# Kernel optimization log

Measured on AMD Instinct MI355X. Metric: run time of the kernel, lower is better.

Reference implementation:

```python
import jax, jax.numpy as jnp
import numpy as np

B, N, D = 8, 8192, 512
WS = 128          # ATTENTION_WINDOW_SIZE
LB = 1            # ATTENTION_WINDOW_LOOKBACK (look_backward)
NW = N // WS      # number of windows (N divisible by WS -> autopad no-op)


def setup_inputs() -> dict:
    key = jax.random.key(0)
    ks = jax.random.split(key, 4)
    s = 0.02
    return {
        "x": jax.random.normal(ks[0], (B, N, D), dtype=jnp.float32),
        "w_q": jax.random.normal(ks[1], (D, D), dtype=jnp.float32) * s,
        "b_q": jnp.zeros((D,), dtype=jnp.float32),
        "w_k": jax.random.normal(ks[2], (D, D), dtype=jnp.float32) * s,
        "b_k": jnp.zeros((D,), dtype=jnp.float32),
        "w_v": jax.random.normal(ks[3], (D, D), dtype=jnp.float32) * s,
        "b_v": jnp.zeros((D,), dtype=jnp.float32),
    }


def _look_around(t, pad_value):
    # t: (B, NW, WS, ...) -> concat of [backward..current] windows along window-length axis
    pad_width = [(0, 0), (LB, 0)] + [(0, 0)] * (t.ndim - 2)
    padded = jnp.pad(t, pad_width, constant_values=pad_value)
    return jnp.concatenate([padded[:, i:i + NW] for i in range(LB + 1)], axis=2)


def _local_attention(q, k, v):
    scale = D ** -0.5
    bq = q.reshape(B, NW, WS, D)
    bk = _look_around(k.reshape(B, NW, WS, D), 0.0)   # (B, NW, (LB+1)*WS, D)
    bv = _look_around(v.reshape(B, NW, WS, D), 0.0)

    # absolute position ticks for causal + padding masks
    tq = jnp.arange(N).reshape(1, NW, WS)                               # query positions
    tk = _look_around(jnp.arange(N).reshape(1, NW, WS), -1)             # key positions, -1 = pad

    sim = jnp.einsum('bwie,bwje->bwij', bq, bk) * scale                 # (B, NW, WS, (LB+1)*WS)
    mask = (tq[..., :, None] < tk[..., None, :]) | (tk[..., None, :] < 0)
    sim = jnp.where(mask, -jnp.finfo(sim.dtype).max, sim)
    attn = jax.nn.softmax(sim, axis=-1)                                  # dropout = 0 -> no-op
    out = jnp.einsum('bwij,bwje->bwie', attn, bv)
    return out.reshape(B, N, D)


def reference(x, w_q, b_q, w_k, b_k, w_v, b_v):
    q = x @ w_q.T + b_q
    k = x @ w_k.T + b_k
    v = x @ w_v.T + b_v
    return _local_attention(q, k, v)
```

## Files before the change

### kernel.cpp

```cpp
#include <hip/hip_runtime.h>


typedef __bf16 bf16x8 __attribute__((ext_vector_type(8)));
typedef float f32x4 __attribute__((ext_vector_type(4)));
typedef unsigned short u16x8 __attribute__((ext_vector_type(8)));

#define BATCH 8
#define SEQ   8192
#define DIM   512
#define NWIN  64
#define TOKS  (BATCH * SEQ)
#define WSELEM ((size_t)TOKS * DIM)

__device__ __forceinline__ unsigned short f2b(float f) {
    union { float f; unsigned int u; } c; c.f = f;
    unsigned int u = c.u;
    return (unsigned short)((u + 0x7FFFu + ((u >> 16) & 1u)) >> 16);
}

__device__ __forceinline__ int swz64(int row, int col) {
    return (row * 64 + col) ^ ((row & 7) << 3);
}
__device__ __forceinline__ int swz128(int row, int col) {
    return (row * 128 + col) ^ ((row & 15) << 3);
}

__device__ __forceinline__ void gload_lds16(const unsigned short* g,
                                            unsigned short* l) {
    __builtin_amdgcn_global_load_lds(
        (const __attribute__((address_space(1))) void*)g,
        (__attribute__((address_space(3))) void*)l, 16, 0, 0);
}

__global__ __launch_bounds__(256) void k_cvt(const float* __restrict__ s,
                                             unsigned short* __restrict__ d,
                                             int n8) {
    const int stride = gridDim.x * blockDim.x;
    for (int i = blockIdx.x * blockDim.x + threadIdx.x; i < n8; i += stride) {
        const float4 a = ((const float4*)s)[2 * i];
        const float4 b = ((const float4*)s)[2 * i + 1];
        u16x8 v;
        v[0] = f2b(a.x); v[1] = f2b(a.y); v[2] = f2b(a.z); v[3] = f2b(a.w);
        v[4] = f2b(b.x); v[5] = f2b(b.y); v[6] = f2b(b.z); v[7] = f2b(b.w);
        ((u16x8*)d)[i] = v;
    }
}

__global__ __launch_bounds__(256, 2) void k_qkv(
    const unsigned short* __restrict__ xb, const unsigned short* __restrict__ wb,
    const float* __restrict__ bq, const float* __restrict__ bk,
    const float* __restrict__ bv,
    unsigned short* __restrict__ qo, unsigned short* __restrict__ ko,
    unsigned short* __restrict__ vto)
{
    __shared__ __align__(16) unsigned short sm[32768];
    unsigned short* Xs = sm;

    int bid = (int)blockIdx.x;
    bid = (bid & 7) * 256 + (bid >> 3);
    const int mt = bid >> 2, nt = bid & 3;
    const int rbase = mt << 7;
    const int cbase = nt << 7;

    const unsigned short* __restrict__ xsrc0 = xb + ((size_t)rbase << 9);
    const unsigned short* __restrict__ wsrc0 = wb + ((size_t)cbase << 9);

    const int tid  = threadIdx.x;
    const int lane = tid & 63;
    const int wid  = tid >> 6;
    const int wm = wid >> 1, wn = wid & 1;
    const int l15 = lane & 15, lg = lane >> 4;

    f32x4 acc[3][4][4];
#pragma unroll
    for (int s = 0; s < 3; ++s)
#pragma unroll
        for (int m = 0; m < 4; ++m)
#pragma unroll
            for (int n = 0; n < 4; ++n) acc[s][m][n] = (f32x4){0.f, 0.f, 0.f, 0.f};

    const int srow = tid >> 3;
    const int gs   = ((tid & 7) ^ (srow & 7)) << 3;
    const int ldso = tid << 3;

    for (int ks = 0; ks < 8; ++ks) {
        const int kc = ks << 6;
#pragma unroll
        for (int i = 0; i < 4; ++i) {
            const int row = (i << 5) + srow;
            gload_lds16(xsrc0 + ((size_t)row << 9) + kc + gs, Xs + (i << 11) + ldso);
        }
#pragma unroll
        for (int ws = 0; ws < 3; ++ws) {
#pragma unroll
            for (int i = 0; i < 4; ++i) {
                const int row = (i << 5) + srow;
                gload_lds16(wsrc0 + ((size_t)ws << 18) + ((size_t)row << 9) + kc + gs,
                            sm + 8192 + (ws << 13) + (i << 11) + ldso);
            }
        }
        __syncthreads();
#pragma unroll
        for (int kk = 0; kk < 64; kk += 32) {
            const int cu = kk + (lg << 3);
            bf16x8 af[4];
#pragma unroll
            for (int m = 0; m < 4; ++m)
                af[m] = *(const bf16x8*)&Xs[swz64((wm << 6) + (m << 4) + l15, cu)];
#pragma unroll
            for (int ws = 0; ws < 3; ++ws) {
                const unsigned short* Wsb = sm + 8192 + (ws << 13);
                bf16x8 bfr[4];
#pragma unroll
                for (int n = 0; n < 4; ++n)
                    bfr[n] = *(const bf16x8*)&Wsb[swz64((wn << 6) + (n << 4) + l15, cu)];
#pragma unroll
                for (int m = 0; m < 4; ++m)
#pragma unroll
                    for (int n = 0; n < 4; ++n)
                        acc[ws][m][n] = __builtin_amdgcn_mfma_f32_16x16x32_bf16(
                            af[m], bfr[n], acc[ws][m][n], 0, 0, 0);
            }
        }
        __syncthreads();
    }

#pragma unroll
    for (int ws = 0; ws < 2; ++ws) {
        unsigned short* __restrict__ out = ws ? ko : qo;
        const float* __restrict__ bias = ws ? bk : bq;
#pragma unroll
        for (int n = 0; n < 4; ++n) {
            const int col = cbase + (wn << 6) + (n << 4) + l15;
            const float bv_ = bias[col];
#pragma unroll
            for (int m = 0; m < 4; ++m)
#pragma unroll
                for (int j = 0; j < 4; ++j) {
                    const int row = rbase + (wm << 6) + (m << 4) + (lg << 2) + j;
                    out[(size_t)row * DIM + col] = f2b(acc[ws][m][n][j] + bv_);
                }
        }
    }
#pragma unroll
    for (int n = 0; n < 4; ++n) {
        const int dv = (wn << 6) + (n << 4) + l15;
        const float bv_ = bv[cbase + dv];
#pragma unroll
        for (int m = 0; m < 4; ++m)
#pragma unroll
            for (int j = 0; j < 4; ++j) {
                const int tok = (wm << 6) + (m << 4) + (lg << 2) + j;
                sm[tok * 129 + dv] = f2b(acc[2][m][n][j] + bv_);
            }
    }
    __syncthreads();
    {
        const int batch = rbase >> 13;
        const int ntok  = rbase & 8191;
        const int dvl0  = tid >> 4;
        const int t16   = (tid & 15) << 3;
#pragma unroll
        for (int p = 0; p < 8; ++p) {
            const int dvl = (p << 4) + dvl0;
            u16x8 v;
#pragma unroll
            for (int j = 0; j < 8; ++j) v[j] = sm[(t16 + j) * 129 + dvl];
            *(u16x8*)&vto[(size_t)batch * (DIM * SEQ)
                          + (size_t)(cbase + dvl) * SEQ + ntok + t16] = v;
        }
    }
}

__global__ __launch_bounds__(512) void k_attn(
    const unsigned short* __restrict__ q,
    const unsigned short* __restrict__ k,
    const unsigned short* __restrict__ vt,
    float* __restrict__ out)
{
    __shared__ __align__(16) unsigned short sm[32768];
    __shared__ float redm[128][4];
    __shared__ float reds[128][4];

    int bid = (int)blockIdx.x;
    bid = (bid & 7) * 64 + (bid >> 3);
    const int b = bid >> 6, w = bid & 63;
    const int tid  = threadIdx.x;
    const int lane = tid & 63, wid = tid >> 6;
    const int l15 = lane & 15, lg = lane >> 4;
    const int wqa = wid >> 2, wka = wid & 3;
    const int kstart = (w - 1) << 7;
    const size_t qrow0 = ((size_t)b << 13) + ((size_t)w << 7);

    f32x4 acc[4][4];
#pragma unroll
    for (int m = 0; m < 4; ++m)
#pragma unroll
        for (int n = 0; n < 4; ++n) acc[m][n] = (f32x4){0.f, 0.f, 0.f, 0.f};

    const int srA = tid >> 4;
    const int gsA = (((tid & 15) ^ (srA & 15)) << 3);

    for (int dstep = 0; dstep < 4; ++dstep) {
        const int dc = dstep << 7;
#pragma unroll
        for (int i = 0; i < 8; ++i) {
            const int r = (i << 5) + srA;
            int krow = kstart + r; krow = krow < 0 ? 0 : krow;
            gload_lds16(k + (((size_t)b << 13) + krow) * DIM + dc + gsA,
                        sm + (i << 12) + (tid << 3));
        }
        __syncthreads();
#pragma unroll
        for (int kk = 0; kk < 128; kk += 32) {
            const int cu = kk + (lg << 3);
            bf16x8 af[4], bf[4];
#pragma unroll
            for (int m = 0; m < 4; ++m) {
                const int rq = (wqa << 6) + (m << 4) + l15;
                af[m] = *(const bf16x8*)&q[(qrow0 + rq) * DIM + dc + cu];
            }
#pragma unroll
            for (int n = 0; n < 4; ++n) {
                const int rk = (wka << 6) + (n << 4) + l15;
                bf[n] = *(const bf16x8*)&sm[swz128(rk, cu)];
            }
#pragma unroll
            for (int m = 0; m < 4; ++m)
#pragma unroll
                for (int n = 0; n < 4; ++n)
                    acc[m][n] = __builtin_amdgcn_mfma_f32_16x16x32_bf16(
                        af[m], bf[n], acc[m][n], 0, 0, 0);
        }
        __syncthreads();
    }

    const float scale = 0.04419417382415922f;
    float pm[4][4];
#pragma unroll
    for (int m = 0; m < 4; ++m)
#pragma unroll
        for (int j = 0; j < 4; ++j) {
            const int qr = (wqa << 6) + (m << 4) + (lg << 2) + j;
            float mx = -3.0e38f;
#pragma unroll
            for (int n = 0; n < 4; ++n) {
                const int c = (wka << 6) + (n << 4) + l15;
                const bool keep = (c <= qr + 128) && (w > 0 || c >= 128);
                const float s = keep ? acc[m][n][j] * scale : -INFINITY;
                acc[m][n][j] = s;
                mx = fmaxf(mx, s);
            }
#pragma unroll
            for (int o = 1; o < 16; o <<= 1) mx = fmaxf(mx, __shfl_xor(mx, o));
            pm[m][j] = mx;
        }
    if (l15 == 0) {
#pragma unroll
        for (int m = 0; m < 4; ++m)
#pragma unroll
            for (int j = 0; j < 4; ++j)
                redm[(wqa << 6) + (m << 4) + (lg << 2) + j][wka] = pm[m][j];
    }
    __syncthreads();

    float ls[4][4];
#pragma unroll
    for (int m = 0; m < 4; ++m)
#pragma unroll
        for (int j = 0; j < 4; ++j) {
            const int qr = (wqa << 6) + (m << 4) + (lg << 2) + j;
            const float g = fmaxf(fmaxf(redm[qr][0], redm[qr][1]),
                                  fmaxf(redm[qr][2], redm[qr][3]));
            float s = 0.f;
#pragma unroll
            for (int n = 0; n < 4; ++n) {
                const float p = __expf(acc[m][n][j] - g);
                acc[m][n][j] = p;
                s += p;
            }
#pragma unroll
            for (int o = 1; o < 16; o <<= 1) s += __shfl_xor(s, o);
            ls[m][j] = s;
        }
    if (l15 == 0) {
#pragma unroll
        for (int m = 0; m < 4; ++m)
#pragma unroll
            for (int j = 0; j < 4; ++j)
                reds[(wqa << 6) + (m << 4) + (lg << 2) + j][wka] = ls[m][j];
    }
    __syncthreads();

#pragma unroll
    for (int m = 0; m < 4; ++m)
#pragma unroll
        for (int j = 0; j < 4; ++j) {
            const int qr = (wqa << 6) + (m << 4) + (lg << 2) + j;
            const float tot = reds[qr][0] + reds[qr][1] + reds[qr][2] + reds[qr][3];
            const float inv = 1.0f / tot;
#pragma unroll
            for (int n = 0; n < 4; ++n) {
                const int c = (wka << 6) + (n << 4) + l15;
                sm[((qr << 8) + c) ^ ((qr & 7) << 3)] = f2b(acc[m][n][j] * inv);
            }
        }
    __syncthreads();

    const int wqb = wid >> 2, wvb = wid & 3;
#pragma unroll
    for (int half = 0; half < 2; ++half) {
        f32x4 oacc[4][4];
#pragma unroll
        for (int m = 0; m < 4; ++m)
#pragma unroll
            for (int n = 0; n < 4; ++n) oacc[m][n] = (f32x4){0.f, 0.f, 0.f, 0.f};
#pragma unroll
        for (int kk = 0; kk < 256; kk += 32) {
            const int klo = kk + (lg << 3);
            bf16x8 af[4], bf[4];
#pragma unroll
            for (int m = 0; m < 4; ++m) {
                const int rq = (wqb << 6) + (m << 4) + l15;
                af[m] = *(const bf16x8*)&sm[((rq << 8) + klo) ^ ((rq & 7) << 3)];
            }
            int key = kstart + klo; key = key < 0 ? 0 : key;
#pragma unroll
            for (int n = 0; n < 4; ++n) {
                const int dv = (half << 8) + (wvb << 6) + (n << 4) + l15;
                bf[n] = *(const bf16x8*)&vt[(((size_t)b * DIM + dv) << 13) + key];
            }
#pragma unroll
            for (int m = 0; m < 4; ++m)
#pragma unroll
                for (int n = 0; n < 4; ++n)
                    oacc[m][n] = __builtin_amdgcn_mfma_f32_16x16x32_bf16(
                        af[m], bf[n], oacc[m][n], 0, 0, 0);
        }
#pragma unroll
        for (int n = 0; n < 4; ++n) {
            const int dv = (half << 8) + (wvb << 6) + (n << 4) + l15;
#pragma unroll
            for (int m = 0; m < 4; ++m)
#pragma unroll
                for (int j = 0; j < 4; ++j) {
                    const int qr = (wqb << 6) + (m << 4) + (lg << 2) + j;
                    out[(qrow0 + qr) * DIM + dv] = oacc[m][n][j];
                }
        }
    }
}

extern "C" void kernel_launch(void* const* d_in, const int* in_sizes, int n_in,
                              void* d_out, int out_size, void* d_ws, size_t ws_size,
                              hipStream_t stream) {
    (void)in_sizes; (void)n_in; (void)out_size; (void)ws_size;
    const float* x  = (const float*)d_in[0];
    const float* wq = (const float*)d_in[1];
    const float* bq = (const float*)d_in[2];
    const float* wk = (const float*)d_in[3];
    const float* bk = (const float*)d_in[4];
    const float* wv = (const float*)d_in[5];
    const float* bv = (const float*)d_in[6];
    float* out = (float*)d_out;

    unsigned short* qws  = (unsigned short*)d_ws;
    unsigned short* kws  = qws + WSELEM;
    unsigned short* vtws = kws + WSELEM;

    unsigned short* xbuf = (unsigned short*)d_out;
    unsigned short* wbuf = xbuf + WSELEM;

    k_cvt<<<2048, 256, 0, stream>>>(x, xbuf, (int)(WSELEM / 8));
    k_cvt<<<128, 256, 0, stream>>>(wq, wbuf, DIM * DIM / 8);
    k_cvt<<<128, 256, 0, stream>>>(wk, wbuf + DIM * DIM, DIM * DIM / 8);
    k_cvt<<<128, 256, 0, stream>>>(wv, wbuf + 2 * DIM * DIM, DIM * DIM / 8);
    k_qkv<<<2048, 256, 0, stream>>>(xbuf, wbuf, bq, bk, bv, qws, kws, vtws);
    k_attn<<<512, 512, 0, stream>>>(qws, kws, vtws, out);
}
```

Measured before the change: 283.3 us.

## Restructure window attention so each wave owns whole query rows, with double-buffered K/V staging

Each wave now computes all 256 key columns for its own 16 query rows. This removes the cross-wave max/sum reductions through shared memory and the barriers that went with them. K tiles are staged into LDS in 64-wide chunks with double buffering. V is written by the projection kernel in a new key-blocked transposed layout, so P·V reads V tiles from double-buffered LDS instead of scattered global loads. Softmax normalization moves to the output store. The risks are heavy register pressure from 128 accumulator floats per lane under launch_bounds(512,2) and a 128 KB LDS footprint.

```diff
diff --git a/kernel.cpp b/kernel.cpp
--- a/kernel.cpp
+++ b/kernel.cpp
@@ -20,9 +20,6 @@
 
 __device__ __forceinline__ int swz64(int row, int col) {
     return (row * 64 + col) ^ ((row & 7) << 3);
-}
-__device__ __forceinline__ int swz128(int row, int col) {
-    return (row * 128 + col) ^ ((row & 15) << 3);
 }
 
 __device__ __forceinline__ void gload_lds16(const unsigned short* g,
@@ -166,21 +163,21 @@
             u16x8 v;
 #pragma unroll
             for (int j = 0; j < 8; ++j) v[j] = sm[(t16 + j) * 129 + dvl];
-            *(u16x8*)&vto[(size_t)batch * (DIM * SEQ)
-                          + (size_t)(cbase + dvl) * SEQ + ntok + t16] = v;
-        }
-    }
-}
-
-__global__ __launch_bounds__(512) void k_attn(
+            const int key0 = ntok + t16;
+            *(u16x8*)&vto[(((size_t)(batch * 256 + (key0 >> 5)) << 9)
+                           + (size_t)(cbase + dvl)) * 32 + (key0 & 31)] = v;
+        }
+    }
+}
+
+__global__ __launch_bounds__(512, 2) void k_attn(
     const unsigned short* __restrict__ q,
     const unsigned short* __restrict__ k,
-    const unsigned short* __restrict__ vt,
+    const unsigned short* __restrict__ vt3,
     float* __restrict__ out)
 {
-    __shared__ __align__(16) unsigned short sm[32768];
-    __shared__ float redm[128][4];
-    __shared__ float reds[128][4];
+    __shared__ __align__(16) unsigned short Kb[32768];
+    __shared__ __align__(16) unsigned short Pl[32768];
 
     int bid = (int)blockIdx.x;
     bid = (bid & 7) * 64 + (bid >> 3);
@@ -188,166 +185,121 @@
     const int tid  = threadIdx.x;
     const int lane = tid & 63, wid = tid >> 6;
     const int l15 = lane & 15, lg = lane >> 4;
-    const int wqa = wid >> 2, wka = wid & 3;
     const int kstart = (w - 1) << 7;
     const size_t qrow0 = ((size_t)b << 13) + ((size_t)w << 7);
-
-    f32x4 acc[4][4];
-#pragma unroll
-    for (int m = 0; m < 4; ++m)
-#pragma unroll
-        for (int n = 0; n < 4; ++n) acc[m][n] = (f32x4){0.f, 0.f, 0.f, 0.f};
-
-    const int srA = tid >> 4;
-    const int gsA = (((tid & 15) ^ (srA & 15)) << 3);
-
-    for (int dstep = 0; dstep < 4; ++dstep) {
-        const int dc = dstep << 7;
-#pragma unroll
-        for (int i = 0; i < 8; ++i) {
-            const int r = (i << 5) + srA;
+    const size_t kbase = (size_t)b << 13;
+
+    const int srow = tid >> 3;
+    const int s0   = tid & 7;
+
+    f32x4 acc[16];
+#pragma unroll
+    for (int n = 0; n < 16; ++n) acc[n] = (f32x4){0.f, 0.f, 0.f, 0.f};
+
+    auto stageK = [&](int buf, int ds) {
+#pragma unroll
+        for (int i = 0; i < 4; ++i) {
+            const int r = (i << 6) + srow;
             int krow = kstart + r; krow = krow < 0 ? 0 : krow;
-            gload_lds16(k + (((size_t)b << 13) + krow) * DIM + dc + gsA,
-                        sm + (i << 12) + (tid << 3));
+            gload_lds16(k + (kbase + krow) * DIM + (ds << 6) + ((s0 ^ (r & 7)) << 3),
+                        Kb + (buf << 14) + (i << 12) + (tid << 3));
+        }
+    };
+
+    stageK(0, 0);
+    stageK(1, 1);
+    __syncthreads();
+    for (int ds = 0; ds < 8; ++ds) {
+        const unsigned short* Kc = Kb + ((ds & 1) << 14);
+#pragma unroll
+        for (int kk2 = 0; kk2 < 2; ++kk2) {
+            const int cu = (kk2 << 5) + (lg << 3);
+            const bf16x8 af = *(const bf16x8*)
+                &q[(qrow0 + (wid << 4) + l15) * DIM + (ds << 6) + cu];
+#pragma unroll
+            for (int n = 0; n < 16; ++n) {
+                const bf16x8 bf = *(const bf16x8*)&Kc[swz64((n << 4) + l15, cu)];
+                acc[n] = __builtin_amdgcn_mfma_f32_16x16x32_bf16(af, bf, acc[n], 0, 0, 0);
+            }
         }
         __syncthreads();
-#pragma unroll
-        for (int kk = 0; kk < 128; kk += 32) {
-            const int cu = kk + (lg << 3);
-            bf16x8 af[4], bf[4];
-#pragma unroll
-            for (int m = 0; m < 4; ++m) {
-                const int rq = (wqa << 6) + (m << 4) + l15;
-                af[m] = *(const bf16x8*)&q[(qrow0 + rq) * DIM + dc + cu];
-            }
-#pragma unroll
-            for (int n = 0; n < 4; ++n) {
-                const int rk = (wka << 6) + (n << 4) + l15;
-                bf[n] = *(const bf16x8*)&sm[swz128(rk, cu)];
-            }
-#pragma unroll
-            for (int m = 0; m < 4; ++m)
-#pragma unroll
-                for (int n = 0; n < 4; ++n)
-                    acc[m][n] = __builtin_amdgcn_mfma_f32_16x16x32_bf16(
-                        af[m], bf[n], acc[m][n], 0, 0, 0);
-        }
-        __syncthreads();
-    }
+        if (ds + 2 < 8) stageK(ds & 1, ds + 2);
+    }
+
+    const int c5base = kstart >> 5;
+    auto stageV = [&](int buf, int kk) {
+        int c5 = c5base + kk; c5 = c5 < 0 ? 0 : c5;
+        const unsigned short* src = vt3 + ((size_t)(b * 256 + c5) << 14);
+#pragma unroll
+        for (int i = 0; i < 4; ++i)
+            gload_lds16(src + (i << 12) + (tid << 3),
+                        Kb + (buf << 14) + (i << 12) + (tid << 3));
+    };
+    stageV(0, 0);
+    stageV(1, 1);
 
     const float scale = 0.04419417382415922f;
-    float pm[4][4];
-#pragma unroll
-    for (int m = 0; m < 4; ++m)
-#pragma unroll
-        for (int j = 0; j < 4; ++j) {
-            const int qr = (wqa << 6) + (m << 4) + (lg << 2) + j;
-            float mx = -3.0e38f;
-#pragma unroll
-            for (int n = 0; n < 4; ++n) {
-                const int c = (wka << 6) + (n << 4) + l15;
-                const bool keep = (c <= qr + 128) && (w > 0 || c >= 128);
-                const float s = keep ? acc[m][n][j] * scale : -INFINITY;
-                acc[m][n][j] = s;
-                mx = fmaxf(mx, s);
-            }
-#pragma unroll
-            for (int o = 1; o < 16; o <<= 1) mx = fmaxf(mx, __shfl_xor(mx, o));
-            pm[m][j] = mx;
-        }
-    if (l15 == 0) {
-#pragma unroll
-        for (int m = 0; m < 4; ++m)
-#pragma unroll
-            for (int j = 0; j < 4; ++j)
-                redm[(wqa << 6) + (m << 4) + (lg << 2) + j][wka] = pm[m][j];
+    float inv[4];
+    unsigned short* Pw = Pl + (wid << 12);
+#pragma unroll
+    for (int jj = 0; jj < 4; ++jj) {
+        const int r  = (lg << 2) + jj;
+        const int qr = (wid << 4) + r;
+        float mx = -3.0e38f;
+#pragma unroll
+        for (int n = 0; n < 16; ++n) {
+            const int c = (n << 4) + l15;
+            const bool keep = (c <= qr + 128) && (w > 0 || c >= 128);
+            const float s = keep ? acc[n][jj] * scale : -INFINITY;
+            acc[n][jj] = s;
+            mx = fmaxf(mx, s);
+        }
+#pragma unroll
+        for (int o = 1; o < 16; o <<= 1) mx = fmaxf(mx, __shfl_xor(mx, o));
+        float sum = 0.f;
+#pragma unroll
+        for (int n = 0; n < 16; ++n) {
+            const float p = __expf(acc[n][jj] - mx);
+            acc[n][jj] = p;
+            sum += p;
+        }
+#pragma unroll
+        for (int o = 1; o < 16; o <<= 1) sum += __shfl_xor(sum, o);
+        inv[jj] = 1.0f / sum;
+#pragma unroll
+        for (int n = 0; n < 16; ++n) {
+            const int c = (n << 4) + l15;
+            Pw[(r << 8) + ((((c >> 3) ^ r) << 3) | (c & 7))] = f2b(acc[n][jj]);
+        }
     }
     __syncthreads();
 
-    float ls[4][4];
-#pragma unroll
-    for (int m = 0; m < 4; ++m)
-#pragma unroll
-        for (int j = 0; j < 4; ++j) {
-            const int qr = (wqa << 6) + (m << 4) + (lg << 2) + j;
-            const float g = fmaxf(fmaxf(redm[qr][0], redm[qr][1]),
-                                  fmaxf(redm[qr][2], redm[qr][3]));
-            float s = 0.f;
-#pragma unroll
-            for (int n = 0; n < 4; ++n) {
-                const float p = __expf(acc[m][n][j] - g);
-                acc[m][n][j] = p;
-                s += p;
-            }
-#pragma unroll
-            for (int o = 1; o < 16; o <<= 1) s += __shfl_xor(s, o);
-            ls[m][j] = s;
-        }
-    if (l15 == 0) {
-#pragma unroll
-        for (int m = 0; m < 4; ++m)
-#pragma unroll
-            for (int j = 0; j < 4; ++j)
-                reds[(wqa << 6) + (m << 4) + (lg << 2) + j][wka] = ls[m][j];
-    }
-    __syncthreads();
-
-#pragma unroll
-    for (int m = 0; m < 4; ++m)
-#pragma unroll
-        for (int j = 0; j < 4; ++j) {
-            const int qr = (wqa << 6) + (m << 4) + (lg << 2) + j;
-            const float tot = reds[qr][0] + reds[qr][1] + reds[qr][2] + reds[qr][3];
-            const float inv = 1.0f / tot;
-#pragma unroll
-            for (int n = 0; n < 4; ++n) {
-                const int c = (wka << 6) + (n << 4) + l15;
-                sm[((qr << 8) + c) ^ ((qr & 7) << 3)] = f2b(acc[m][n][j] * inv);
-            }
-        }
-    __syncthreads();
-
-    const int wqb = wid >> 2, wvb = wid & 3;
-#pragma unroll
-    for (int half = 0; half < 2; ++half) {
-        f32x4 oacc[4][4];
-#pragma unroll
-        for (int m = 0; m < 4; ++m)
-#pragma unroll
-            for (int n = 0; n < 4; ++n) oacc[m][n] = (f32x4){0.f, 0.f, 0.f, 0.f};
-#pragma unroll
-        for (int kk = 0; kk < 256; kk += 32) {
-            const int klo = kk + (lg << 3);
-            bf16x8 af[4], bf[4];
-#pragma unroll
-            for (int m = 0; m < 4; ++m) {
-                const int rq = (wqb << 6) + (m << 4) + l15;
-                af[m] = *(const bf16x8*)&sm[((rq << 8) + klo) ^ ((rq & 7) << 3)];
-            }
-            int key = kstart + klo; key = key < 0 ? 0 : key;
-#pragma unroll
-            for (int n = 0; n < 4; ++n) {
-                const int dv = (half << 8) + (wvb << 6) + (n << 4) + l15;
-                bf[n] = *(const bf16x8*)&vt[(((size_t)b * DIM + dv) << 13) + key];
-            }
-#pragma unroll
-            for (int m = 0; m < 4; ++m)
-#pragma unroll
-                for (int n = 0; n < 4; ++n)
-                    oacc[m][n] = __builtin_amdgcn_mfma_f32_16x16x32_bf16(
-                        af[m], bf[n], oacc[m][n], 0, 0, 0);
-        }
-#pragma unroll
-        for (int n = 0; n < 4; ++n) {
-            const int dv = (half << 8) + (wvb << 6) + (n << 4) + l15;
-#pragma unroll
-            for (int m = 0; m < 4; ++m)
-#pragma unroll
-                for (int j = 0; j < 4; ++j) {
-                    const int qr = (wqb << 6) + (m << 4) + (lg << 2) + j;
-                    out[(qrow0 + qr) * DIM + dv] = oacc[m][n][j];
-                }
-        }
+    f32x4 oacc[32];
+#pragma unroll
+    for (int n = 0; n < 32; ++n) oacc[n] = (f32x4){0.f, 0.f, 0.f, 0.f};
+
+    for (int kk = 0; kk < 8; ++kk) {
+        const unsigned short* Vc = Kb + ((kk & 1) << 14);
+        const bf16x8 pa = *(const bf16x8*)
+            &Pw[(l15 << 8) + ((((kk << 2) + lg) ^ l15) << 3)];
+#pragma unroll
+        for (int n = 0; n < 32; ++n) {
+            const bf16x8 bv_ = *(const bf16x8*)&Vc[(((n << 4) + l15) << 5) + (lg << 3)];
+            oacc[n] = __builtin_amdgcn_mfma_f32_16x16x32_bf16(pa, bv_, oacc[n], 0, 0, 0);
+        }
+        if (kk < 7) {
+            __syncthreads();
+            if (kk + 2 < 8) stageV(kk & 1, kk + 2);
+        }
+    }
+
+#pragma unroll
+    for (int n = 0; n < 32; ++n) {
+        const int dv = (n << 4) + l15;
+        float* orow = out + (qrow0 + (wid << 4) + (lg << 2)) * DIM + dv;
+#pragma unroll
+        for (int jj = 0; jj < 4; ++jj)
+            orow[(size_t)jj * DIM] = oacc[n][jj] * inv[jj];
     }
 }
 
```

Measured after the change: 238.5 us. -15.8%, faster.
